# Performance work log

Measured on AMD Instinct MI355X. Metric: run time of the kernel, lower is better.

Reference implementation:

```python
import jax, jax.numpy as jnp
import numpy as np

N_NODES = 20000
IN_FEAT = 128
CONV_OUT = 32
N_EDGES = 640000
FC1_OUT = 128


def setup_inputs() -> dict:
    key = jax.random.key(0)
    ks = jax.random.split(key, 8)
    x = jax.random.normal(ks[0], (N_NODES, IN_FEAT), dtype=jnp.float32)
    edge_index = jax.random.randint(ks[1], (2, N_EDGES), 0, N_NODES, dtype=jnp.int64)
    # GCNConv params (PyG: lin weight [in, out] applied as x @ W, plus bias)
    w_conv = jax.random.normal(ks[2], (IN_FEAT, CONV_OUT), dtype=jnp.float32) * (1.0 / np.sqrt(IN_FEAT))
    b_conv = jnp.zeros((CONV_OUT,), dtype=jnp.float32)
    # fc1: Linear(32*N -> 128), torch stores weight as [out, in]
    w_fc1 = jax.random.normal(ks[3], (FC1_OUT, CONV_OUT * N_NODES), dtype=jnp.float32) * (1.0 / np.sqrt(CONV_OUT * N_NODES))
    b_fc1 = jnp.zeros((FC1_OUT,), dtype=jnp.float32)
    # fc2: Linear(128 -> N)
    w_fc2 = jax.random.normal(ks[4], (N_NODES, FC1_OUT), dtype=jnp.float32) * (1.0 / np.sqrt(FC1_OUT))
    b_fc2 = jnp.zeros((N_NODES,), dtype=jnp.float32)
    return {"x": x, "edge_index": edge_index, "w_conv": w_conv, "b_conv": b_conv,
            "w_fc1": w_fc1, "b_fc1": b_fc1, "w_fc2": w_fc2, "b_fc2": b_fc2}


def gcn_conv(x, edge_index, w, b):
    # PyG GCNConv default: add self-loops, symmetric normalization D^-1/2 (A+I) D^-1/2
    n = x.shape[0]
    loop = jnp.arange(n, dtype=edge_index.dtype)
    src = jnp.concatenate([edge_index[0], loop])  # [E+N]
    dst = jnp.concatenate([edge_index[1], loop])
    deg = jax.ops.segment_sum(jnp.ones_like(dst, dtype=x.dtype), dst, num_segments=n)
    dinv = jnp.where(deg > 0, jax.lax.rsqrt(deg), 0.0)
    norm = dinv[src] * dinv[dst]  # [E+N]
    h = x @ w  # [N, out] — transform before propagate
    msg = h[src] * norm[:, None]  # gather
    agg = jax.ops.segment_sum(msg, dst, num_segments=n)  # scatter-add
    return agg + b


def reference(x, edge_index, w_conv, b_conv, w_fc1, b_fc1, w_fc2, b_fc2):
    h1 = jax.nn.relu(gcn_conv(x, edge_index, w_conv, b_conv))  # [N, 32]; dropout inactive (eval)
    flat = h1.reshape(-1, CONV_OUT * N_NODES)  # [1, 32*N]
    h3 = jax.nn.relu(flat @ w_fc1.T + b_fc1)   # [1, 128]
    out = jax.nn.relu(h3 @ w_fc2.T + b_fc2)    # [1, N] q-values
    return out
```

## Files before the change

kernel.cpp:

```cpp
#include <hip/hip_runtime.h>

#define N_NODES 20000
#define IN_FEAT 128
#define CONV_OUT 32
#define N_EDGES 640000
#define FC1_OUT 128


#define ZERO_WORDS 20128

__global__ __launch_bounds__(256) void k_zero(float4* __restrict__ p) {
    int i = blockIdx.x * 256 + threadIdx.x;
    if (i < ZERO_WORDS / 4) p[i] = make_float4(0.f, 0.f, 0.f, 0.f);
}

__global__ __launch_bounds__(256) void k_degslot(const int* __restrict__ ei,
                                                 int* __restrict__ cnt,
                                                 int* __restrict__ r) {
    int e = blockIdx.x * 256 + threadIdx.x;
    if (e < N_EDGES) {
        int d = ei[N_EDGES + e];
        r[e] = atomicAdd(&cnt[d], 1);
    }
}

#define SCAN_T 1024
#define SCAN_CHUNK 20
__global__ __launch_bounds__(1024) void k_scan(const int* __restrict__ cnt,
                                               int* __restrict__ startv,
                                               float* __restrict__ dinv) {
    __shared__ int ld[SCAN_T * SCAN_CHUNK];
    __shared__ int ps[SCAN_T];
    int t = threadIdx.x;
    const int4* c4 = (const int4*)cnt;
    int4* l4 = (int4*)ld;
    #pragma unroll
    for (int i = 0; i < 5; ++i) {
        int idx = i * SCAN_T + t;
        l4[idx] = (idx < N_NODES / 4) ? c4[idx] : make_int4(0, 0, 0, 0);
    }
    __syncthreads();
    int local[SCAN_CHUNK];
    int base = t * SCAN_CHUNK;
    int sum = 0;
    #pragma unroll
    for (int i = 0; i < SCAN_CHUNK; ++i) { local[i] = ld[base + i]; sum += local[i]; }
    ps[t] = sum;
    __syncthreads();
    for (int off = 1; off < SCAN_T; off <<= 1) {
        int v = (t >= off) ? ps[t - off] : 0;
        __syncthreads();
        ps[t] += v;
        __syncthreads();
    }
    int run = (t == 0) ? 0 : ps[t - 1];
    #pragma unroll
    for (int i = 0; i < SCAN_CHUNK; ++i) {
        int n = base + i;
        ld[n] = run;
        if (n < N_NODES) dinv[n] = rsqrtf((float)local[i] + 1.0f);
        run += local[i];
    }
    __syncthreads();
    int4* s4 = (int4*)startv;
    #pragma unroll
    for (int i = 0; i < 5; ++i) {
        int idx = i * SCAN_T + t;
        if (idx < N_NODES / 4) s4[idx] = l4[idx];
    }
    if (t == 0) startv[N_NODES] = N_EDGES;
}

__global__ __launch_bounds__(256) void k_gemm1(const float* __restrict__ x,
                                               const float* __restrict__ w,
                                               const float* __restrict__ dinv,
                                               float* __restrict__ h) {
    __shared__ float xs[64][132];
    __shared__ float ws[128][32];
    int tid = threadIdx.x;
    int n0 = blockIdx.x * 64;

    const float4* w4 = (const float4*)w;
    float4* ws4 = (float4*)ws;
    #pragma unroll
    for (int i = 0; i < 4; ++i) ws4[i * 256 + tid] = w4[i * 256 + tid];

    const float4* x4 = (const float4*)x;
    #pragma unroll
    for (int i = 0; i < 8; ++i) {
        int idx = i * 256 + tid;
        int nl  = idx >> 5;
        int k4  = idx & 31;
        int n   = n0 + nl;
        float4 v = make_float4(0.f, 0.f, 0.f, 0.f);
        if (n < N_NODES) v = x4[(size_t)n * 32 + k4];
        *(float4*)&xs[nl][k4 * 4] = v;
    }
    __syncthreads();

    int c4  = tid & 7;
    int nl0 = tid >> 3;
    const float4* wsrow = (const float4*)ws;
    #pragma unroll
    for (int p = 0; p < 2; ++p) {
        int nl = nl0 + p * 32;
        float4 acc = make_float4(0.f, 0.f, 0.f, 0.f);
        #pragma unroll 8
        for (int k = 0; k < 128; k += 4) {
            float4 xv  = *(const float4*)&xs[nl][k];
            float4 wv0 = wsrow[(k + 0) * 8 + c4];
            float4 wv1 = wsrow[(k + 1) * 8 + c4];
            float4 wv2 = wsrow[(k + 2) * 8 + c4];
            float4 wv3 = wsrow[(k + 3) * 8 + c4];
            acc.x += xv.x * wv0.x + xv.y * wv1.x + xv.z * wv2.x + xv.w * wv3.x;
            acc.y += xv.x * wv0.y + xv.y * wv1.y + xv.z * wv2.y + xv.w * wv3.y;
            acc.z += xv.x * wv0.z + xv.y * wv1.z + xv.z * wv2.z + xv.w * wv3.z;
            acc.w += xv.x * wv0.w + xv.y * wv1.w + xv.z * wv2.w + xv.w * wv3.w;
        }
        int n = n0 + nl;
        if (n < N_NODES) {
            float dv = dinv[n];
            acc.x *= dv; acc.y *= dv; acc.z *= dv; acc.w *= dv;
            *(float4*)&h[(size_t)n * 32 + c4 * 4] = acc;
        }
    }
}

__global__ __launch_bounds__(256) void k_fill(const int* __restrict__ ei,
                                              const int* __restrict__ startv,
                                              const int* __restrict__ r,
                                              int* __restrict__ csr) {
    int e = blockIdx.x * 256 + threadIdx.x;
    if (e < N_EDGES) {
        int s = ei[e];
        int d = ei[N_EDGES + e];
        csr[startv[d] + r[e]] = s;
    }
}

__global__ __launch_bounds__(256) void k_gather(const int* __restrict__ startv,
                                                const int* __restrict__ csr,
                                                const float* __restrict__ h,
                                                const float* __restrict__ dinv,
                                                const float* __restrict__ bc,
                                                float* __restrict__ flat) {
    int tid  = threadIdx.x;
    int lane = tid & 63;
    int n    = blockIdx.x * 4 + (tid >> 6);
    if (n >= N_NODES) return;
    int es = lane >> 3;
    int f4 = lane & 7;
    const float4* h4 = (const float4*)h;
    float4 acc = make_float4(0.f, 0.f, 0.f, 0.f);
    int p0 = startv[n], p1 = startv[n + 1];
    #pragma unroll 2
    for (int p = p0 + es; p < p1; p += 8) {
        int s = csr[p];
        float4 v = h4[(size_t)s * 8 + f4];
        acc.x += v.x; acc.y += v.y; acc.z += v.z; acc.w += v.w;
    }
    #pragma unroll
    for (int m = 8; m < 64; m <<= 1) {
        acc.x += __shfl_xor(acc.x, m);
        acc.y += __shfl_xor(acc.y, m);
        acc.z += __shfl_xor(acc.z, m);
        acc.w += __shfl_xor(acc.w, m);
    }
    if (lane < 8) {
        float4 self = h4[(size_t)n * 8 + f4];
        float dv = dinv[n];
        float4 b = ((const float4*)bc)[f4];
        float4 r_;
        r_.x = fmaxf((acc.x + self.x) * dv + b.x, 0.f);
        r_.y = fmaxf((acc.y + self.y) * dv + b.y, 0.f);
        r_.z = fmaxf((acc.z + self.z) * dv + b.z, 0.f);
        r_.w = fmaxf((acc.w + self.w) * dv + b.w, 0.f);
        ((float4*)flat)[(size_t)n * 8 + f4] = r_;
    }
}

__global__ __launch_bounds__(256) void k_fc1(const float* __restrict__ flat,
                                             const float* __restrict__ w,
                                             float* __restrict__ h3pre) {
    int bid = blockIdx.x;
    int j  = bid & 127;
    int ch = bid >> 7;
    const float4* w4 = (const float4*)(w + (size_t)j * (CONV_OUT * N_NODES));
    const float4* f4 = (const float4*)flat;
    int base = ch * 6400;
    float acc = 0.f;
    #pragma unroll 5
    for (int it = 0; it < 25; ++it) {
        int k = base + it * 256 + threadIdx.x;
        float4 wv = w4[k];
        float4 fv = f4[k];
        acc += wv.x * fv.x + wv.y * fv.y + wv.z * fv.z + wv.w * fv.w;
    }
    #pragma unroll
    for (int o = 32; o > 0; o >>= 1) acc += __shfl_down(acc, o);
    __shared__ float red[4];
    if ((threadIdx.x & 63) == 0) red[threadIdx.x >> 6] = acc;
    __syncthreads();
    if (threadIdx.x == 0) atomicAdd(&h3pre[j], red[0] + red[1] + red[2] + red[3]);
}

__global__ __launch_bounds__(256) void k_fc2(const float* __restrict__ h3pre,
                                             const float* __restrict__ b1,
                                             const float* __restrict__ w2,
                                             const float* __restrict__ b2,
                                             float* __restrict__ out) {
    __shared__ float4 h3s[32];
    int tid = threadIdx.x;
    if (tid < 32) {
        float4 v;
        v.x = fmaxf(h3pre[tid * 4 + 0] + b1[tid * 4 + 0], 0.f);
        v.y = fmaxf(h3pre[tid * 4 + 1] + b1[tid * 4 + 1], 0.f);
        v.z = fmaxf(h3pre[tid * 4 + 2] + b1[tid * 4 + 2], 0.f);
        v.w = fmaxf(h3pre[tid * 4 + 3] + b1[tid * 4 + 3], 0.f);
        h3s[tid] = v;
    }
    __syncthreads();
    int i = blockIdx.x * 256 + tid;
    if (i < N_NODES) {
        const float4* wr = (const float4*)(w2 + (size_t)i * FC1_OUT);
        float acc = b2[i];
        #pragma unroll
        for (int j = 0; j < 32; ++j) {
            float4 wv = wr[j];
            float4 hv = h3s[j];
            acc += wv.x * hv.x + wv.y * hv.y + wv.z * hv.z + wv.w * hv.w;
        }
        out[i] = fmaxf(acc, 0.f);
    }
}

extern "C" void kernel_launch(void* const* d_in, const int* in_sizes, int n_in,
                              void* d_out, int out_size, void* d_ws, size_t ws_size,
                              hipStream_t stream) {
    const float* x      = (const float*)d_in[0];
    const int*   ei     = (const int*)d_in[1];
    const float* w_conv = (const float*)d_in[2];
    const float* b_conv = (const float*)d_in[3];
    const float* w_fc1  = (const float*)d_in[4];
    const float* b_fc1  = (const float*)d_in[5];
    const float* w_fc2  = (const float*)d_in[6];
    const float* b_fc2  = (const float*)d_in[7];
    float* ws = (float*)d_ws;
    int*   cnt    = (int*)ws;
    float* h3pre  = ws + 20000;
    int*   startv = (int*)(ws + 20128);
    float* dinv   = ws + 40132;
    int*   r      = (int*)(ws + 60132);
    int*   csr    = (int*)(ws + 700132);
    float* h      = ws + 1340132;
    float* flat   = ws + 1980132;
    float* out    = (float*)d_out;

    k_zero<<<(ZERO_WORDS / 4 + 255) / 256, 256, 0, stream>>>((float4*)d_ws);
    k_degslot<<<(N_EDGES + 255) / 256, 256, 0, stream>>>(ei, cnt, r);
    k_scan<<<1, SCAN_T, 0, stream>>>(cnt, startv, dinv);
    k_gemm1<<<(N_NODES + 63) / 64, 256, 0, stream>>>(x, w_conv, dinv, h);
    k_fill<<<(N_EDGES + 255) / 256, 256, 0, stream>>>(ei, startv, r, csr);
    k_gather<<<(N_NODES + 3) / 4, 256, 0, stream>>>(startv, csr, h, dinv, b_conv, flat);
    k_fc1<<<128 * 25, 256, 0, stream>>>(flat, w_fc1, h3pre);
    k_fc2<<<(N_NODES + 255) / 256, 256, 0, stream>>>(h3pre, b_fc1, w_fc2, b_fc2, out);
}
```

Measured before the change: 164.9 us.

## Compute four fc1 outputs per block and replace atomics with partial-sum buffer

Each fc1 block now computes four output neurons at once, reusing each loaded flat vector chunk across four weight rows, which cuts the number of times the activation vector is read. Per-chunk partial sums are written to a buffer and reduced in fc2 instead of using atomicAdd, so the zeroing pass shrinks. The launch count drops from 3200 to 800 blocks, and each thread carries more loads in flight, which may lower occupancy or parallelism on a bandwidth-bound weight stream.

```diff
diff --git a/kernel.cpp b/kernel.cpp
--- a/kernel.cpp
+++ b/kernel.cpp
@@ -7,7 +7,7 @@
 #define FC1_OUT 128
 
 
-#define ZERO_WORDS 20128
+#define ZERO_WORDS 20000
 
 __global__ __launch_bounds__(256) void k_zero(float4* __restrict__ p) {
     int i = blockIdx.x * 256 + threadIdx.x;
@@ -179,55 +179,78 @@
     }
 }
 
+#define FC1_CH 25
 __global__ __launch_bounds__(256) void k_fc1(const float* __restrict__ flat,
                                              const float* __restrict__ w,
-                                             float* __restrict__ h3pre) {
+                                             float* __restrict__ part) {
     int bid = blockIdx.x;
-    int j  = bid & 127;
-    int ch = bid >> 7;
-    const float4* w4 = (const float4*)(w + (size_t)j * (CONV_OUT * N_NODES));
+    int jg = bid & 31;
+    int ch = bid >> 5;
+    int j0 = jg * 4;
     const float4* f4 = (const float4*)flat;
+    const float4* w0 = (const float4*)(w + (size_t)(j0 + 0) * (CONV_OUT * N_NODES));
+    const float4* w1 = (const float4*)(w + (size_t)(j0 + 1) * (CONV_OUT * N_NODES));
+    const float4* w2 = (const float4*)(w + (size_t)(j0 + 2) * (CONV_OUT * N_NODES));
+    const float4* w3 = (const float4*)(w + (size_t)(j0 + 3) * (CONV_OUT * N_NODES));
     int base = ch * 6400;
-    float acc = 0.f;
+    float a0 = 0.f, a1 = 0.f, a2 = 0.f, a3 = 0.f;
     #pragma unroll 5
     for (int it = 0; it < 25; ++it) {
         int k = base + it * 256 + threadIdx.x;
-        float4 wv = w4[k];
-        float4 fv = f4[k];
-        acc += wv.x * fv.x + wv.y * fv.y + wv.z * fv.z + wv.w * fv.w;
-    }
-    #pragma unroll
-    for (int o = 32; o > 0; o >>= 1) acc += __shfl_down(acc, o);
-    __shared__ float red[4];
-    if ((threadIdx.x & 63) == 0) red[threadIdx.x >> 6] = acc;
-    __syncthreads();
-    if (threadIdx.x == 0) atomicAdd(&h3pre[j], red[0] + red[1] + red[2] + red[3]);
-}
-
-__global__ __launch_bounds__(256) void k_fc2(const float* __restrict__ h3pre,
+        float4 fv  = f4[k];
+        float4 v0  = w0[k];
+        float4 v1  = w1[k];
+        float4 v2  = w2[k];
+        float4 v3  = w3[k];
+        a0 += v0.x * fv.x + v0.y * fv.y + v0.z * fv.z + v0.w * fv.w;
+        a1 += v1.x * fv.x + v1.y * fv.y + v1.z * fv.z + v1.w * fv.w;
+        a2 += v2.x * fv.x + v2.y * fv.y + v2.z * fv.z + v2.w * fv.w;
+        a3 += v3.x * fv.x + v3.y * fv.y + v3.z * fv.z + v3.w * fv.w;
+    }
+    #pragma unroll
+    for (int o = 32; o > 0; o >>= 1) {
+        a0 += __shfl_down(a0, o);
+        a1 += __shfl_down(a1, o);
+        a2 += __shfl_down(a2, o);
+        a3 += __shfl_down(a3, o);
+    }
+    __shared__ float red[4][4];
+    int wv = threadIdx.x >> 6;
+    if ((threadIdx.x & 63) == 0) {
+        red[wv][0] = a0; red[wv][1] = a1; red[wv][2] = a2; red[wv][3] = a3;
+    }
+    __syncthreads();
+    if (threadIdx.x < 4) {
+        float s = red[0][threadIdx.x] + red[1][threadIdx.x] +
+                  red[2][threadIdx.x] + red[3][threadIdx.x];
+        part[(size_t)(j0 + threadIdx.x) * FC1_CH + ch] = s;
+    }
+}
+
+__global__ __launch_bounds__(256) void k_fc2(const float* __restrict__ part,
                                              const float* __restrict__ b1,
                                              const float* __restrict__ w2,
                                              const float* __restrict__ b2,
                                              float* __restrict__ out) {
-    __shared__ float4 h3s[32];
+    __shared__ float h3s[128];
     int tid = threadIdx.x;
-    if (tid < 32) {
-        float4 v;
-        v.x = fmaxf(h3pre[tid * 4 + 0] + b1[tid * 4 + 0], 0.f);
-        v.y = fmaxf(h3pre[tid * 4 + 1] + b1[tid * 4 + 1], 0.f);
-        v.z = fmaxf(h3pre[tid * 4 + 2] + b1[tid * 4 + 2], 0.f);
-        v.w = fmaxf(h3pre[tid * 4 + 3] + b1[tid * 4 + 3], 0.f);
-        h3s[tid] = v;
+    if (tid < 128) {
+        const float* p = part + (size_t)tid * FC1_CH;
+        float s = 0.f;
+        #pragma unroll
+        for (int i = 0; i < FC1_CH; ++i) s += p[i];
+        h3s[tid] = fmaxf(s + b1[tid], 0.f);
     }
     __syncthreads();
     int i = blockIdx.x * 256 + tid;
     if (i < N_NODES) {
         const float4* wr = (const float4*)(w2 + (size_t)i * FC1_OUT);
+        const float4* h4 = (const float4*)h3s;
         float acc = b2[i];
         #pragma unroll
         for (int j = 0; j < 32; ++j) {
             float4 wv = wr[j];
-            float4 hv = h3s[j];
+            float4 hv = h4[j];
             acc += wv.x * hv.x + wv.y * hv.y + wv.z * hv.z + wv.w * hv.w;
         }
         out[i] = fmaxf(acc, 0.f);
@@ -247,13 +270,13 @@
     const float* b_fc2  = (const float*)d_in[7];
     float* ws = (float*)d_ws;
     int*   cnt    = (int*)ws;
-    float* h3pre  = ws + 20000;
-    int*   startv = (int*)(ws + 20128);
-    float* dinv   = ws + 40132;
-    int*   r      = (int*)(ws + 60132);
-    int*   csr    = (int*)(ws + 700132);
-    float* h      = ws + 1340132;
-    float* flat   = ws + 1980132;
+    float* part   = ws + 20000;
+    int*   startv = (int*)(ws + 23200);
+    float* dinv   = ws + 43204;
+    int*   r      = (int*)(ws + 63204);
+    int*   csr    = (int*)(ws + 703204);
+    float* h      = ws + 1343204;
+    float* flat   = ws + 1983204;
     float* out    = (float*)d_out;
 
     k_zero<<<(ZERO_WORDS / 4 + 255) / 256, 256, 0, stream>>>((float4*)d_ws);
@@ -262,6 +285,6 @@
     k_gemm1<<<(N_NODES + 63) / 64, 256, 0, stream>>>(x, w_conv, dinv, h);
     k_fill<<<(N_EDGES + 255) / 256, 256, 0, stream>>>(ei, startv, r, csr);
     k_gather<<<(N_NODES + 3) / 4, 256, 0, stream>>>(startv, csr, h, dinv, b_conv, flat);
-    k_fc1<<<128 * 25, 256, 0, stream>>>(flat, w_fc1, h3pre);
-    k_fc2<<<(N_NODES + 255) / 256, 256, 0, stream>>>(h3pre, b_fc1, w_fc2, b_fc2, out);
-}
+    k_fc1<<<32 * FC1_CH, 256, 0, stream>>>(flat, w_fc1, part);
+    k_fc2<<<(N_NODES + 255) / 256, 256, 0, stream>>>(part, b_fc1, w_fc2, b_fc2, out);
+}
```

New measurement: 165.7 us. Within noise of the previous version (+0.5%).
